# Kernel optimization log

Hardware: AMD Instinct MI355X
Metric: run time of the kernel (lower is better)

Reference implementation:

```python
import jax, jax.numpy as jnp
import numpy as np

B, S, D, H, DH, E, DFF = 8, 512, 768, 12, 64, 8, 3072
EPS = 1e-12
SCALE = D ** -0.5  # note: original scales by hidden_size**-0.5, not head_dim


def _ln(x, g, b):
    m = x.mean(-1, keepdims=True)
    v = ((x - m) ** 2).mean(-1, keepdims=True)
    return (x - m) * jax.lax.rsqrt(v + EPS) * g + b


def _expert(x, mask, Wqkv_e, Wd_e, bd_e, g1, be1, W1_e, b1_e, W2_e, b2_e, g2, be2):
    b, s, d = x.shape
    # fused per-head QKV: (B,S,D) x (H,3*DH,D) -> (B,H,S,3*DH)
    qkv = jnp.einsum('bnd,hkd->bhnk', x, Wqkv_e)
    q, k, v = jnp.split(qkv, 3, axis=-1)  # each (B,H,S,DH)
    scores = jnp.einsum('bhid,bhjd->bhij', q, k) * SCALE
    scores = jnp.where(mask[:, None, None, :] == 0, -jnp.inf, scores)
    attn = jax.nn.softmax(scores, axis=-1)
    ctx = jnp.einsum('bhij,bhjd->bhid', attn, v)
    ctx = ctx.transpose(0, 2, 1, 3).reshape(b, s, d)  # concat heads
    att = ctx @ Wd_e.T + bd_e              # attention.dense output (pre-residual)
    feat = att.mean(axis=1)                # (B,D) routing feature (mean over seq)
    h = _ln(att + x, g1, be1)              # post-norm attention block
    ffn = jax.nn.gelu(h @ W1_e.T + b1_e, approximate=False) @ W2_e.T + b2_e
    out = _ln(h + ffn, g2, be2)            # post-norm FFN block (dropout = eval/identity)
    return out, feat


def setup_inputs() -> dict:
    key = jax.random.key(0)
    ks = jax.random.split(key, 8)
    s = 0.02
    return {
        'hidden_states': jax.random.normal(ks[0], (B, S, D), jnp.float32),
        'attention_mask': jnp.ones((B, S), jnp.int32),
        'Wqkv': jax.random.normal(ks[1], (E, H, 3 * DH, D), jnp.float32) * s,
        'Wd': jax.random.normal(ks[2], (E, D, D), jnp.float32) * s,
        'bd': jnp.zeros((E, D), jnp.float32),
        'ln1_g': jnp.ones((E, D), jnp.float32),
        'ln1_b': jnp.zeros((E, D), jnp.float32),
        'W1': jax.random.normal(ks[3], (E, DFF, D), jnp.float32) * s,
        'b1': jnp.zeros((E, DFF), jnp.float32),
        'W2': jax.random.normal(ks[4], (E, D, DFF), jnp.float32) * s,
        'b2': jnp.zeros((E, D), jnp.float32),
        'ln2_g': jnp.ones((E, D), jnp.float32),
        'ln2_b': jnp.zeros((E, D), jnp.float32),
        'centers': jax.random.normal(ks[5], (E, D), jnp.float32) * 0.1,
    }


def reference(hidden_states, attention_mask, Wqkv, Wd, bd, ln1_g, ln1_b,
              W1, b1, W2, b2, ln2_g, ln2_b, centers):
    outs, feats = [], []
    for e in range(centers.shape[0]):  # small fixed set of experts
        o, f = _expert(hidden_states, attention_mask, Wqkv[e], Wd[e], bd[e],
                       ln1_g[e], ln1_b[e], W1[e], b1[e], W2[e], b2[e],
                       ln2_g[e], ln2_b[e])
        outs.append(o)
        feats.append(f)
    outs = jnp.stack(outs)    # (E,B,S,D)
    feats = jnp.stack(feats)  # (E,B,D)
    dists = jnp.linalg.norm(feats - centers[:, None, :], axis=-1)  # (E,B) torch.dist
    sel = jnp.argmin(dists, axis=0)  # (B,) hard routing
    return outs[sel, jnp.arange(outs.shape[1])]  # (B,S,D)
```

## Files before the change

kernel.cpp:

```cpp
#include <hip/hip_runtime.h>
#include <hip/hip_fp16.h>
#include <math.h>
#include <stdint.h>

#define Bb 8
#define Ss 512
#define Dd 768
#define Hh 12
#define Ee 8
#define DFF 3072
#define MROWS 4096
#define QKVN 2304

static __device__ const float SCALE_ = 0.036084391824351615f;

typedef short bf8_t __attribute__((ext_vector_type(8)));
typedef _Float16 f16x4_t __attribute__((ext_vector_type(4)));
typedef float f32x4_t __attribute__((ext_vector_type(4)));

__device__ __forceinline__ float bf2f(unsigned short u){
  union { unsigned int i; float f; } x; x.i = ((unsigned int)u)<<16; return x.f;
}
__device__ __forceinline__ unsigned short f2bf(float f){
  union { float f; unsigned int i; } x; x.f = f;
  unsigned int u = x.i;
  return (unsigned short)((u + 0x7fffu + ((u>>16)&1u)) >> 16);
}

__device__ __forceinline__ void gl_lds16(const void* g, void* l){
  __builtin_amdgcn_global_load_lds(
      (const __attribute__((address_space(1))) unsigned int*)(g),
      (__attribute__((address_space(3))) unsigned int*)(uintptr_t)(l),
      16, 0, 0);
}

__global__ void cast_kernel(const float* __restrict__ in, unsigned short* __restrict__ out, int n){
  int i = (blockIdx.x*256 + threadIdx.x)*4;
  if (i >= n) return;
  const float4 v = *(const float4*)(in + i);
  ushort4 o; o.x=f2bf(v.x); o.y=f2bf(v.y); o.z=f2bf(v.z); o.w=f2bf(v.w);
  *(ushort4*)(out + i) = o;
}

template<int MODE>
__global__ __launch_bounds__(256)
void gemm_bt(const unsigned short* __restrict__ A,
             const unsigned short* __restrict__ Bbf,
             const float* __restrict__ Bf32,
             const float* __restrict__ bias,
             void* __restrict__ Cout,
             int K, int N,
             long bStrideZ, long cStrideZ,
             const int* __restrict__ sel,
             long selAStride, long selBStride, int selBiasStride,
             int swz)
{
  constexpr int BP = (MODE >= 2) ? 40 : 32;
  __shared__ unsigned short As[128*32];
  __shared__ unsigned short Bs[128*BP];

  int rt, ct, zz;
  if (swz == 1) {
    const int id = (blockIdx.z*gridDim.y + blockIdx.y)*gridDim.x + blockIdx.x;
    const int xcd = id & 7, slot = id >> 3;
    zz = xcd; ct = slot % gridDim.x; rt = slot / gridDim.x;
  } else if (swz == 2) {
    const int id = blockIdx.y*gridDim.x + blockIdx.x;
    const int xcd = id & 7, slot = id >> 3;
    rt = xcd*4 + (slot & 3); ct = slot >> 2; zz = 0;
  } else {
    rt = blockIdx.y; ct = blockIdx.x; zz = blockIdx.z;
  }

  const int t = threadIdx.x;
  const int w = t>>6, l = t&63, q4 = l>>4, mr = l&15;
  const int wm = (w&1)*64, wn = (w>>1)*64;
  const int sr = t>>2, cv = t&3;

  const unsigned short* Ap = A;
  const unsigned short* Bp = Bbf;
  const float* Bf_ = Bf32;
  const float* biasp = bias;
  if (MODE == 0) {
    Bp += (size_t)zz * bStrideZ;
  } else {
    const int ex = sel[rt>>2];
    if (MODE == 1) { Ap += (size_t)ex * selAStride; Bp += (size_t)ex * selBStride; }
    else           { Bf_ += (size_t)ex * selBStride; }
    biasp += (long)ex * selBiasStride;
  }

  f32x4_t acc[4][4];
  #pragma unroll
  for (int i=0;i<4;i++)
    #pragma unroll
    for (int j=0;j<4;j++) acc[i][j] = (f32x4_t){0.f,0.f,0.f,0.f};

  const unsigned short* gA = Ap + (size_t)(rt*128 + w*16 + (l>>2))*K + (l&3)*8;
  unsigned short* lA = As + w*512;
  const unsigned short* gB = nullptr;
  unsigned short* lB = Bs + w*512;
  if (MODE < 2) gB = Bp + (size_t)(ct*128 + w*16 + (l>>2))*K + (l&3)*8;

  for (int k0 = 0; k0 < K; k0 += 32) {
    uint4 b0, b1;
    if (MODE >= 2) {
      const float* Br0 = Bf_ + (long)(ct*128 + sr)*K + cv*8 + k0;
      const float* Br1 = Br0 + (long)64*K;
      float4 f0a = *(const float4*)Br0;  float4 f0b = *(const float4*)(Br0+4);
      float4 f1a = *(const float4*)Br1;  float4 f1b = *(const float4*)(Br1+4);
      union { unsigned short s[8]; uint4 v; } p0, p1;
      p0.s[0]=f2bf(f0a.x); p0.s[1]=f2bf(f0a.y); p0.s[2]=f2bf(f0a.z); p0.s[3]=f2bf(f0a.w);
      p0.s[4]=f2bf(f0b.x); p0.s[5]=f2bf(f0b.y); p0.s[6]=f2bf(f0b.z); p0.s[7]=f2bf(f0b.w);
      p1.s[0]=f2bf(f1a.x); p1.s[1]=f2bf(f1a.y); p1.s[2]=f2bf(f1a.z); p1.s[3]=f2bf(f1a.w);
      p1.s[4]=f2bf(f1b.x); p1.s[5]=f2bf(f1b.y); p1.s[6]=f2bf(f1b.z); p1.s[7]=f2bf(f1b.w);
      b0 = p0.v; b1 = p1.v;
    }
    __syncthreads();
    gl_lds16(gA + k0,                lA);
    gl_lds16(gA + (size_t)64*K + k0, lA + 2048);
    if (MODE < 2) {
      gl_lds16(gB + k0,                lB);
      gl_lds16(gB + (size_t)64*K + k0, lB + 2048);
    } else {
      *(uint4*)&Bs[sr*40 + cv*8]      = b0;
      *(uint4*)&Bs[(sr+64)*40 + cv*8] = b1;
    }
    __syncthreads();
    bf8_t af[4], bfv[4];
    #pragma unroll
    for (int i=0;i<4;i++) af[i]  = *(const bf8_t*)&As[(wm+i*16+mr)*32 + q4*8];
    #pragma unroll
    for (int j=0;j<4;j++) bfv[j] = *(const bf8_t*)&Bs[(wn+j*16+mr)*BP + q4*8];
    #pragma unroll
    for (int i=0;i<4;i++)
      #pragma unroll
      for (int j=0;j<4;j++)
        acc[i][j] = __builtin_amdgcn_mfma_f32_16x16x32_bf16(af[i], bfv[j], acc[i][j], 0,0,0);
  }

  const long Cld = N;
  unsigned short* Cb16 = (unsigned short*)Cout + (size_t)zz * cStrideZ;
  float* Cf32 = (float*)Cout;
  #pragma unroll
  for (int j=0;j<4;j++){
    const int n = ct*128 + wn + j*16 + mr;
    const float bv = (MODE==0) ? 0.f : biasp[n];
    #pragma unroll
    for (int i=0;i<4;i++){
      const long mbase = (long)rt*128 + wm + i*16 + q4*4;
      #pragma unroll
      for (int r=0;r<4;r++){
        const float v = acc[i][j][r] + bv;
        const long m = mbase + r;
        if (MODE==0 || MODE==1) {
          Cb16[m*Cld + n] = f2bf(v);
        } else if (MODE==2) {
          const float g = 0.5f*v*(1.0f + erff(v*0.70710678118654752f));
          Cb16[m*Cld + n] = f2bf(g);
        } else {
          Cf32[m*Cld + n] = v;
        }
      }
    }
  }
}

__global__ __launch_bounds__(256)
void attn_kernel(const unsigned short* __restrict__ qkv,
                 const int* __restrict__ mask,
                 unsigned short* __restrict__ ctx,
                 long qkvStrideZ, long ctxStrideZ)
{
  const int qb = blockIdx.x, h = blockIdx.y;
  const int zz = blockIdx.z;
  const int b = zz & 7, e = zz >> 3;
  qkv += (size_t)e * qkvStrideZ;
  ctx += (size_t)e * ctxStrideZ;

  const int t = threadIdx.x, w = t>>6, l = t&63, q4 = l>>4, mr = l&15;
  __shared__ unsigned short Ks[16*72];
  __shared__ unsigned short Vs[64*20];

  const int srow = b*512 + qb*64 + w*16;
  const unsigned short* qp = qkv + (long)(srow+mr)*QKVN + h*192;
  const bf8_t qf0 = *(const bf8_t*)(qp + q4*8);
  const bf8_t qf1 = *(const bf8_t*)(qp + 32 + q4*8);

  f32x4_t cacc[4];
  #pragma unroll
  for (int d=0; d<4; d++) cacc[d] = (f32x4_t){0.f,0.f,0.f,0.f};
  float lsum = 0.f;

  const int el   = t*4;
  const int skey = el>>6;
  const int sd   = el&63;

  for (int kt=0; kt<32; kt++){
    const long krow = (long)(b*512 + kt*16 + skey)*QKVN + h*192;
    const uint2 kv = *(const uint2*)(qkv + krow + 64  + sd);
    const uint2 vv = *(const uint2*)(qkv + krow + 128 + sd);
    __syncthreads();
    *(uint2*)&Ks[skey*72 + sd] = kv;
    {
      const unsigned short* pv = (const unsigned short*)&vv;
      #pragma unroll
      for (int jj=0;jj<4;jj++){
        const __half hv = __float2half(bf2f(pv[jj]));
        Vs[(sd+jj)*20 + skey] = __half_as_ushort(hv);
      }
    }
    __syncthreads();

    const bf8_t kf0 = *(const bf8_t*)&Ks[mr*72 + q4*8];
    const bf8_t kf1 = *(const bf8_t*)&Ks[mr*72 + 32 + q4*8];
    f32x4_t st = __builtin_amdgcn_mfma_f32_16x16x32_bf16(kf0, qf0, (f32x4_t){0.f,0.f,0.f,0.f}, 0,0,0);
    st = __builtin_amdgcn_mfma_f32_16x16x32_bf16(kf1, qf1, st, 0,0,0);

    f16x4_t pf;
    #pragma unroll
    for (int r=0;r<4;r++){
      const int key = kt*16 + q4*4 + r;
      float p = __expf(st[r]*SCALE_);
      if (mask[b*512 + key] == 0) p = 0.f;
      lsum += p;
      pf[r] = (_Float16)p;
    }
    #pragma unroll
    for (int dblk=0; dblk<4; dblk++){
      const f16x4_t vf = *(const f16x4_t*)&Vs[(dblk*16+mr)*20 + q4*4];
      cacc[dblk] = __builtin_amdgcn_mfma_f32_16x16x16f16(pf, vf, cacc[dblk], 0,0,0);
    }
  }

  lsum += __shfl_xor(lsum, 16);
  lsum += __shfl_xor(lsum, 32);
  #pragma unroll
  for (int r=0;r<4;r++){
    const int m2 = q4*4 + r;
    const float lr = __shfl(lsum, m2);
    const float inv = 1.0f/lr;
    const long orow = (long)(b*512 + qb*64 + w*16 + m2)*Dd + h*64;
    #pragma unroll
    for (int dblk=0; dblk<4; dblk++){
      ctx[orow + dblk*16 + mr] = f2bf(cacc[dblk][r]*inv);
    }
  }
}

__global__ void ctxmean_kernel(const unsigned short* __restrict__ ctx, float* __restrict__ out){
  const int d = blockIdx.x*256 + threadIdx.x;
  const int b = blockIdx.y, e = blockIdx.z;
  const unsigned short* p = ctx + ((size_t)e*MROWS + b*512)*Dd + d;
  float s = 0.f;
  for (int i=0;i<512;i++) s += bf2f(p[(size_t)i*Dd]);
  out[((size_t)e*Bb + b)*Dd + d] = s * (1.0f/512.0f);
}

__global__ __launch_bounds__(256)
void featgemm_kernel(const float* __restrict__ ctxmean, const unsigned short* __restrict__ Wdb,
                     const float* __restrict__ bd, float* __restrict__ feat){
  __shared__ float xs[Dd];
  const int b = blockIdx.x, e = blockIdx.y;
  const int t = threadIdx.x;
  for (int i=t;i<Dd;i+=256) xs[i] = ctxmean[((size_t)e*Bb+b)*Dd + i];
  __syncthreads();
  #pragma unroll
  for (int c0=0;c0<3;c0++){
    const int col = c0*256 + t;
    const unsigned short* wr = Wdb + ((size_t)e*Dd + col)*Dd;
    float s = 0.f;
    for (int k=0;k<Dd;k+=8){
      bf8_t wv = *(const bf8_t*)(wr + k);
      const unsigned short* wp = (const unsigned short*)&wv;
      #pragma unroll
      for (int j=0;j<8;j++) s += bf2f(wp[j]) * xs[k+j];
    }
    feat[((size_t)e*Bb+b)*Dd + col] = s + bd[(size_t)e*Dd + col];
  }
}

__global__ void routing_kernel(const float* __restrict__ feat, const float* __restrict__ centers,
                               int* __restrict__ sel)
{
  __shared__ float d2s[64];
  const int t = threadIdx.x;
  if (t < 64){
    const int e = t>>3, b = t&7;
    const float* f = feat + (long)(e*Bb + b)*Dd;
    const float* c = centers + (long)e*Dd;
    float s = 0.f;
    for (int d=0; d<Dd; d++){
      const float df = f[d] - c[d];
      s += df*df;
    }
    d2s[t] = s;
  }
  __syncthreads();
  if (t < 8){
    float best = 3.4e38f; int bi = 0;
    for (int e=0;e<8;e++){ const float v = d2s[e*8+t]; if (v < best){ best=v; bi=e; } }
    sel[t] = bi;
  }
}

__global__ __launch_bounds__(256)
void hprep_kernel(const unsigned short* __restrict__ attsel, const float* __restrict__ x,
                  const float* __restrict__ g, const float* __restrict__ be,
                  const int* __restrict__ sel, unsigned short* __restrict__ hbuf)
{
  const int w = threadIdx.x>>6, l = threadIdx.x&63;
  const int row = blockIdx.x*4 + w;
  const int b = row>>9;
  const int e = sel[b];
  const unsigned short* ap = attsel + (long)row*Dd;
  const float* xp = x + (long)row*Dd;
  float v[12]; float s = 0.f;
  #pragma unroll
  for (int i=0;i<12;i++){ const int d = i*64 + l; v[i] = bf2f(ap[d]) + xp[d]; s += v[i]; }
  #pragma unroll
  for (int o=32;o>0;o>>=1) s += __shfl_xor(s, o);
  const float mean = s * (1.0f/768.0f);
  float vs = 0.f;
  #pragma unroll
  for (int i=0;i<12;i++){ const float dd = v[i]-mean; vs += dd*dd; }
  #pragma unroll
  for (int o=32;o>0;o>>=1) vs += __shfl_xor(vs, o);
  const float rs = rsqrtf(vs*(1.0f/768.0f) + 1e-12f);
  #pragma unroll
  for (int i=0;i<12;i++){
    const int d = i*64 + l;
    hbuf[(long)row*Dd + d] = f2bf((v[i]-mean)*rs*g[(long)e*Dd+d] + be[(long)e*Dd+d]);
  }
}

__global__ __launch_bounds__(256)
void ln2_kernel(const unsigned short* __restrict__ hbuf, const float* __restrict__ tbuf,
                const float* __restrict__ g, const float* __restrict__ be,
                const int* __restrict__ sel, float* __restrict__ out)
{
  const int w = threadIdx.x>>6, l = threadIdx.x&63;
  const int row = blockIdx.x*4 + w;
  const int b = row>>9;
  const int e = sel[b];
  const unsigned short* hp = hbuf + (long)row*Dd;
  const float* tp = tbuf + (long)row*Dd;
  float v[12]; float s = 0.f;
  #pragma unroll
  for (int i=0;i<12;i++){ const int d = i*64 + l; v[i] = bf2f(hp[d]) + tp[d]; s += v[i]; }
  #pragma unroll
  for (int o=32;o>0;o>>=1) s += __shfl_xor(s, o);
  const float mean = s * (1.0f/768.0f);
  float vs = 0.f;
  #pragma unroll
  for (int i=0;i<12;i++){ const float dd = v[i]-mean; vs += dd*dd; }
  #pragma unroll
  for (int o=32;o>0;o>>=1) vs += __shfl_xor(vs, o);
  const float rs = rsqrtf(vs*(1.0f/768.0f) + 1e-12f);
  #pragma unroll
  for (int i=0;i<12;i++){
    const int d = i*64 + l;
    out[(long)row*Dd + d] = (v[i]-mean)*rs*g[(long)e*Dd+d] + be[(long)e*Dd+d];
  }
}

extern "C" void kernel_launch(void* const* d_in, const int* in_sizes, int n_in,
                              void* d_out, int out_size, void* d_ws, size_t ws_size,
                              hipStream_t stream)
{
  const float* x      = (const float*)d_in[0];
  const int*   mask   = (const int*)d_in[1];
  const float* Wqkv   = (const float*)d_in[2];
  const float* Wd     = (const float*)d_in[3];
  const float* bd     = (const float*)d_in[4];
  const float* ln1g   = (const float*)d_in[5];
  const float* ln1b   = (const float*)d_in[6];
  const float* W1     = (const float*)d_in[7];
  const float* b1     = (const float*)d_in[8];
  const float* W2     = (const float*)d_in[9];
  const float* b2     = (const float*)d_in[10];
  const float* ln2g   = (const float*)d_in[11];
  const float* ln2b   = (const float*)d_in[12];
  const float* centers= (const float*)d_in[13];

  int zc;
  if      (ws_size >= 258347264ull) zc = 8;
  else if (ws_size >= 182849792ull) zc = 4;
  else if (ws_size >= 145101056ull) zc = 2;
  else                              zc = 1;

  char* p = (char*)d_ws;
  auto carve = [&](size_t bytes)->char*{ char* r = p; p += ((bytes + 255) & ~(size_t)255); return r; };

  unsigned short* xb      = (unsigned short*)carve((size_t)MROWS*Dd*2);
  unsigned short* Wqkvb   = (unsigned short*)carve((size_t)Ee*QKVN*Dd*2);
  unsigned short* Wdb     = (unsigned short*)carve((size_t)Ee*Dd*Dd*2);
  float*          ctxmean = (float*)carve((size_t)Ee*Bb*Dd*4);
  float*          feat    = (float*)carve((size_t)Ee*Bb*Dd*4);
  int*            sel     = (int*)carve(256);
  unsigned short* hbuf    = (unsigned short*)carve((size_t)MROWS*Dd*2);
  unsigned short* attsel  = (unsigned short*)carve((size_t)MROWS*Dd*2);
  unsigned short* qkvchk  = (unsigned short*)carve((size_t)zc*MROWS*QKVN*2);
  unsigned short* ctx_all = (unsigned short*)carve((size_t)Ee*MROWS*Dd*2);
  unsigned short* Gbuf = attsel;
  float*          tbuf = (float*)ctx_all;

  cast_kernel<<<(MROWS*Dd/4 + 255)/256, 256, 0, stream>>>(x, xb, MROWS*Dd);
  cast_kernel<<<(Ee*QKVN*Dd/4 + 255)/256, 256, 0, stream>>>(Wqkv, Wqkvb, Ee*QKVN*Dd);
  cast_kernel<<<(Ee*Dd*Dd/4 + 255)/256, 256, 0, stream>>>(Wd, Wdb, Ee*Dd*Dd);

  const int nchunk = Ee / zc;
  for (int c = 0; c < nchunk; c++){
    gemm_bt<0><<<dim3(QKVN/128, MROWS/128, zc), 256, 0, stream>>>(
        xb, Wqkvb + (size_t)c*zc*QKVN*Dd, nullptr, nullptr, qkvchk,
        Dd, QKVN, (long)QKVN*Dd, (long)MROWS*QKVN,
        nullptr, 0, 0, 0, (zc==8) ? 1 : 0);
    attn_kernel<<<dim3(8, Hh, Bb*zc), 256, 0, stream>>>(
        qkvchk, mask, ctx_all + (size_t)c*zc*MROWS*Dd,
        (long)MROWS*QKVN, (long)MROWS*Dd);
    ctxmean_kernel<<<dim3(3, Bb, zc), 256, 0, stream>>>(
        ctx_all + (size_t)c*zc*MROWS*Dd, ctxmean + (size_t)c*zc*Bb*Dd);
  }

  featgemm_kernel<<<dim3(Bb, Ee), 256, 0, stream>>>(ctxmean, Wdb, bd, feat);
  routing_kernel<<<1, 64, 0, stream>>>(feat, centers, sel);

  gemm_bt<1><<<dim3(Dd/128, MROWS/128, 1), 256, 0, stream>>>(
      ctx_all, Wdb, nullptr, bd, attsel, Dd, Dd, 0, 0,
      sel, (long)MROWS*Dd, (long)Dd*Dd, Dd, 2);

  hprep_kernel<<<MROWS/4, 256, 0, stream>>>(attsel, x, ln1g, ln1b, sel, hbuf);
  gemm_bt<2><<<dim3(DFF/128, MROWS/128, 1), 256, 0, stream>>>(
      hbuf, nullptr, W1, b1, Gbuf, Dd, DFF, 0, 0,
      sel, 0, (long)DFF*Dd, DFF, 2);
  gemm_bt<3><<<dim3(Dd/128, MROWS/128, 1), 256, 0, stream>>>(
      Gbuf, nullptr, W2, b2, tbuf, DFF, Dd, 0, 0,
      sel, 0, (long)Dd*DFF, Dd, 2);
  ln2_kernel<<<MROWS/4, 256, 0, stream>>>(hbuf, tbuf, ln2g, ln2b, sel, (float*)d_out);
}
```

Baseline: 822.2 us.

## Replace QKV GEMM with 256x256 tile, 8-wave, ping-pong pipelined kernel

```diff
diff --git a/kernel.cpp b/kernel.cpp
--- a/kernel.cpp
+++ b/kernel.cpp
@@ -40,6 +40,152 @@
   const float4 v = *(const float4*)(in + i);
   ushort4 o; o.x=f2bf(v.x); o.y=f2bf(v.y); o.z=f2bf(v.z); o.w=f2bf(v.w);
   *(ushort4*)(out + i) = o;
+}
+
+#define VMW6 asm volatile("s_waitcnt vmcnt(6)" ::: "memory")
+#define VMW0 asm volatile("s_waitcnt vmcnt(0)" ::: "memory")
+#define NOOP ((void)0)
+
+#define STG_A(SL,H,KT) { char* d_ = smem + (SL)*32768 + (H)*16384 + w*1024;          \
+    gl_lds16(aSrc[0] + (size_t)(H)*hK + (size_t)(KT)*64, d_);                        \
+    gl_lds16(aSrc[1] + (size_t)(H)*hK + (size_t)(KT)*64, d_ + 8192); }
+#define STG_B(SL,H,KT) { char* d_ = smem + 65536 + (SL)*32768 + (H)*16384 + w*1024;  \
+    gl_lds16(bSrc[0] + (size_t)(H)*hK + (size_t)(KT)*64, d_);                        \
+    gl_lds16(bSrc[1] + (size_t)(H)*hK + (size_t)(KT)*64, d_ + 8192); }
+
+#define PHASE(SL, QM, QN, DO_A, STAGE, WAITC)                                        \
+  {                                                                                  \
+    STAGE;                                                                           \
+    WAITC;                                                                           \
+    __builtin_amdgcn_s_barrier();                                                    \
+    asm volatile("" ::: "memory");                                                   \
+    if (DO_A) {                                                                      \
+      _Pragma("unroll") for (int i_=0;i_<4;i_++)                                     \
+        _Pragma("unroll") for (int k_=0;k_<2;k_++)                                   \
+          afr[i_][k_] = *(const bf8_t*)(smem + (SL)*32768 + (QM)*16384 + aoff[i_][k_]); \
+    }                                                                                \
+    _Pragma("unroll") for (int j_=0;j_<2;j_++)                                       \
+      _Pragma("unroll") for (int k_=0;k_<2;k_++)                                     \
+        bfr[j_][k_] = *(const bf8_t*)(smem + (SL)*32768 + (QN)*16384 + boff[j_][k_]); \
+    asm volatile("s_waitcnt lgkmcnt(0)" ::: "memory");                               \
+    __builtin_amdgcn_sched_barrier(0);                                               \
+    __builtin_amdgcn_s_setprio(1);                                                   \
+    _Pragma("unroll") for (int k_=0;k_<2;k_++)                                       \
+      _Pragma("unroll") for (int i_=0;i_<4;i_++)                                     \
+        _Pragma("unroll") for (int j_=0;j_<2;j_++)                                   \
+          acc[QM][QN][i_][j_] = __builtin_amdgcn_mfma_f32_16x16x32_bf16(             \
+              afr[i_][k_], bfr[j_][k_], acc[QM][QN][i_][j_], 0,0,0);                 \
+    __builtin_amdgcn_s_setprio(0);                                                   \
+    __builtin_amdgcn_s_barrier();                                                    \
+  }
+
+__global__ __launch_bounds__(512, 2)
+void gemm8p(const unsigned short* __restrict__ A,
+            const unsigned short* __restrict__ B,
+            unsigned short* __restrict__ C,
+            int K, int N, long bStrideZ, long cStrideZ, int swz)
+{
+  extern __shared__ char smem[];
+  const int t = threadIdx.x;
+  const int w = t>>6, l = t&63, q4 = l>>4, mr = l&15;
+  const int wm = w>>2, wn = w&3;
+
+  int ct, rt, zz;
+  if (swz == 1) {
+    const int id = (blockIdx.z*gridDim.y + blockIdx.y)*gridDim.x + blockIdx.x;
+    const int xcd = id & 7, slot = id >> 3;
+    zz = xcd; ct = slot % gridDim.x; rt = slot / gridDim.x;
+  } else { ct = blockIdx.x; rt = blockIdx.y; zz = blockIdx.z; }
+
+  const unsigned short* Ap = A + (size_t)rt*256*K;
+  const unsigned short* Bp = B + (size_t)zz*bStrideZ + (size_t)ct*256*K;
+
+  const unsigned short* aSrc[2];
+  const unsigned short* bSrc[2];
+  #pragma unroll
+  for (int c=0;c<2;c++){
+    const int o  = c*8192 + t*16;
+    const int lb = o ^ (((o>>7)&7)<<4);
+    const int row = lb>>7, kcol = (lb&127)>>1;
+    aSrc[c] = Ap + (size_t)row*K + kcol;
+    bSrc[c] = Bp + (size_t)row*K + kcol;
+  }
+  const size_t hK = (size_t)128*K;
+
+  int aoff[4][2], boff[2][2];
+  #pragma unroll
+  for (int i=0;i<4;i++)
+    #pragma unroll
+    for (int kk=0;kk<2;kk++){
+      const int row = wm*64 + i*16 + mr;
+      int b_ = row*128 + kk*64 + q4*16;
+      b_ ^= (row&7)<<4;
+      aoff[i][kk] = b_;
+    }
+  #pragma unroll
+  for (int j=0;j<2;j++)
+    #pragma unroll
+    for (int kk=0;kk<2;kk++){
+      const int row = wn*32 + j*16 + mr;
+      int b_ = row*128 + kk*64 + q4*16;
+      b_ ^= (row&7)<<4;
+      boff[j][kk] = 65536 + b_;
+    }
+
+  f32x4_t acc[2][2][4][2];
+  #pragma unroll
+  for (int a0=0;a0<2;a0++)
+    #pragma unroll
+    for (int a1=0;a1<2;a1++)
+      #pragma unroll
+      for (int a2=0;a2<4;a2++)
+        #pragma unroll
+        for (int a3=0;a3<2;a3++) acc[a0][a1][a2][a3] = (f32x4_t){0.f,0.f,0.f,0.f};
+
+  bf8_t afr[4][2], bfr[2][2];
+
+  STG_A(0,0,0); STG_A(0,1,0); STG_B(0,0,0); STG_B(0,1,0);
+  STG_A(1,0,1); STG_B(1,1,1);
+
+  const int NITER = K >> 7;
+  for (int it = 0; it < NITER-1; ++it){
+    const int t1 = 2*it+1, t2 = 2*it+2, t3 = 2*it+3;
+    PHASE(0,0,0, 1, STG_A(1,1,t1), VMW6);
+    PHASE(0,0,1, 0, STG_B(1,0,t1), NOOP);
+    PHASE(0,1,1, 1, STG_A(0,0,t2), NOOP);
+    PHASE(0,1,0, 0, STG_B(0,1,t2), NOOP);
+    PHASE(1,0,0, 1, STG_A(0,1,t2), VMW6);
+    PHASE(1,0,1, 0, STG_B(0,0,t2), NOOP);
+    PHASE(1,1,1, 1, STG_A(1,0,t3), NOOP);
+    PHASE(1,1,0, 0, STG_B(1,1,t3), NOOP);
+  }
+  {
+    const int t1 = 2*NITER-1;
+    PHASE(0,0,0, 1, STG_A(1,1,t1), VMW6);
+    PHASE(0,0,1, 0, STG_B(1,0,t1), NOOP);
+    PHASE(0,1,1, 1, NOOP, NOOP);
+    PHASE(0,1,0, 0, NOOP, NOOP);
+    PHASE(1,0,0, 1, NOOP, VMW0);
+    PHASE(1,0,1, 0, NOOP, NOOP);
+    PHASE(1,1,1, 1, NOOP, NOOP);
+    PHASE(1,1,0, 0, NOOP, NOOP);
+  }
+
+  unsigned short* Cp = C + (size_t)zz*cStrideZ;
+  #pragma unroll
+  for (int qm=0;qm<2;qm++)
+    #pragma unroll
+    for (int qn=0;qn<2;qn++)
+      #pragma unroll
+      for (int i=0;i<4;i++)
+        #pragma unroll
+        for (int j=0;j<2;j++){
+          const long mb = (long)rt*256 + qm*128 + wm*64 + i*16 + q4*4;
+          const long n  = (long)ct*256 + qn*128 + wn*32 + j*16 + mr;
+          #pragma unroll
+          for (int r=0;r<4;r++)
+            Cp[(mb+r)*N + n] = f2bf(acc[qm][qn][i][j][r]);
+        }
 }
 
 template<int MODE>
@@ -383,6 +529,8 @@
   const float* ln2b   = (const float*)d_in[12];
   const float* centers= (const float*)d_in[13];
 
+  hipFuncSetAttribute((const void*)gemm8p, hipFuncAttributeMaxDynamicSharedMemorySize, 131072);
+
   int zc;
   if      (ws_size >= 258347264ull) zc = 8;
   else if (ws_size >= 182849792ull) zc = 4;
@@ -411,10 +559,9 @@
 
   const int nchunk = Ee / zc;
   for (int c = 0; c < nchunk; c++){
-    gemm_bt<0><<<dim3(QKVN/128, MROWS/128, zc), 256, 0, stream>>>(
-        xb, Wqkvb + (size_t)c*zc*QKVN*Dd, nullptr, nullptr, qkvchk,
-        Dd, QKVN, (long)QKVN*Dd, (long)MROWS*QKVN,
-        nullptr, 0, 0, 0, (zc==8) ? 1 : 0);
+    gemm8p<<<dim3(QKVN/256, MROWS/256, zc), 512, 131072, stream>>>(
+        xb, Wqkvb + (size_t)c*zc*QKVN*Dd, qkvchk,
+        Dd, QKVN, (long)QKVN*Dd, (long)MROWS*QKVN, (zc==8) ? 1 : 0);
     attn_kernel<<<dim3(8, Hh, Bb*zc), 256, 0, stream>>>(
         qkvchk, mask, ctx_all + (size_t)c*zc*MROWS*Dd,
         (long)MROWS*QKVN, (long)MROWS*Dd);
```

New measurement: 785.6 us. 1.05x faster.
